# Kernel tuning notes

Hardware: AMD Instinct MI355X
Metric: run time of the kernel (lower is better)

Reference implementation:

```python
import jax, jax.numpy as jnp
import numpy as np

D_MODEL = 1024
N_HEADS = 16
HEAD_DIM = D_MODEL // N_HEADS
SCALE = float(np.sqrt(HEAD_DIM))


def setup_inputs() -> dict:
    key = jax.random.key(0)
    ks = jax.random.split(key, 12)
    B, S, D = 4, 2048, D_MODEL
    std = 1.0 / np.sqrt(D)
    inp = {
        "query": jax.random.normal(ks[0], (B, S, D), jnp.float32),
        "key": jax.random.normal(ks[1], (B, S, D), jnp.float32),
        "value": jax.random.normal(ks[2], (B, S, D), jnp.float32),
        "wq_w": jax.random.normal(ks[3], (D, D), jnp.float32) * std,
        "wq_b": jnp.zeros((D,), jnp.float32),
        "wk_w": jax.random.normal(ks[4], (D, D), jnp.float32) * std,
        "wk_b": jnp.zeros((D,), jnp.float32),
        "wv_w": jax.random.normal(ks[5], (D, D), jnp.float32) * std,
        "wv_b": jnp.zeros((D,), jnp.float32),
        "fc_w": jax.random.normal(ks[6], (D, D), jnp.float32) * std,
        "fc_b": jnp.zeros((D,), jnp.float32),
    }
    return inp


def reference(query, key, value, wq_w, wq_b, wk_w, wk_b, wv_w, wv_b, fc_w, fc_b):
    B, S, D = query.shape
    H, Hd = N_HEADS, HEAD_DIM
    # QKV projections (torch Linear: x @ W.T + b)
    Q = query @ wq_w.T + wq_b
    K = key @ wk_w.T + wk_b
    V = value @ wv_w.T + wv_b
    # [B, H, S, Hd]
    Q = Q.reshape(B, S, H, Hd).transpose(0, 2, 1, 3)
    K = K.reshape(B, S, H, Hd).transpose(0, 2, 1, 3)
    V = V.reshape(B, S, H, Hd).transpose(0, 2, 1, 3)
    energy = jnp.einsum("bhqd,bhkd->bhqk", Q, K) / SCALE
    attention = jax.nn.softmax(energy, axis=-1)  # dropout=0 (eval)
    weighted = jnp.einsum("bhqk,bhkd->bhqd", attention, V)
    weighted = weighted.transpose(0, 2, 1, 3).reshape(B, S, D)
    output = weighted @ fc_w.T + fc_b
    return (output, attention)
```

## Files before the change

### kernel.cpp

```cpp
#include <hip/hip_runtime.h>
#include <hip/hip_bf16.h>
#include <math.h>

typedef __attribute__((ext_vector_type(8))) short short8;
typedef __attribute__((ext_vector_type(4))) short short4v;
typedef __attribute__((ext_vector_type(4))) float float4v;
typedef __attribute__((ext_vector_type(2))) unsigned int uint2v;

#define GLD_LDS(g, l) __builtin_amdgcn_global_load_lds( \
    (const __attribute__((address_space(1))) void*)(g), \
    (__attribute__((address_space(3))) void*)(l), 16, 0, 0)

__device__ __forceinline__ short f2bf(float x) {
  __hip_bfloat16 h = __float2bfloat16(x);
  return __builtin_bit_cast(short, h);
}

__device__ __forceinline__ float fexp2(float x) {
  return __builtin_amdgcn_exp2f(x);
}

__global__ __launch_bounds__(256) void cast3(
    const float4v* __restrict__ in0, const float4v* __restrict__ in1,
    const float4v* __restrict__ in2,
    short4v* __restrict__ o0, short4v* __restrict__ o1, short4v* __restrict__ o2,
    int n4)
{
  const float4v* in = blockIdx.y == 0 ? in0 : blockIdx.y == 1 ? in1 : in2;
  short4v* out = blockIdx.y == 0 ? o0 : blockIdx.y == 1 ? o1 : o2;
  int i = blockIdx.x * 256 + threadIdx.x;
  if (i < n4) {
    float4v v = in[i];
    short4v o;
    o[0] = f2bf(v[0]); o[1] = f2bf(v[1]); o[2] = f2bf(v[2]); o[3] = f2bf(v[3]);
    out[i] = o;
  }
}

__global__ __launch_bounds__(256) void cast4(
    const float4v* __restrict__ in0, const float4v* __restrict__ in1,
    const float4v* __restrict__ in2, const float4v* __restrict__ in3,
    short4v* __restrict__ o0, short4v* __restrict__ o1,
    short4v* __restrict__ o2, short4v* __restrict__ o3,
    int n4)
{
  const float4v* in = blockIdx.y == 0 ? in0 : blockIdx.y == 1 ? in1
                    : blockIdx.y == 2 ? in2 : in3;
  short4v* out = blockIdx.y == 0 ? o0 : blockIdx.y == 1 ? o1
               : blockIdx.y == 2 ? o2 : o3;
  int i = blockIdx.x * 256 + threadIdx.x;
  if (i < n4) {
    float4v v = in[i];
    short4v o;
    o[0] = f2bf(v[0]); o[1] = f2bf(v[1]); o[2] = f2bf(v[2]); o[3] = f2bf(v[3]);
    out[i] = o;
  }
}

template<int MODE>
__global__ __launch_bounds__(256) void gemm_bt(
    const short* __restrict__ A0, const short* __restrict__ B0,
    const float* __restrict__ bias0, void* __restrict__ Cv0,
    const short* __restrict__ A1, const short* __restrict__ B1,
    const float* __restrict__ bias1, void* __restrict__ Cv1,
    int M, int N, int K)
{
  const short* A = blockIdx.z ? A1 : A0;
  const short* B = blockIdx.z ? B1 : B0;
  const float* bias = blockIdx.z ? bias1 : bias0;
  void* Cv = blockIdx.z ? Cv1 : Cv0;

  __shared__ short As[2][128 * 64];
  __shared__ short Bs[2][128 * 64];
  const int tid = threadIdx.x;
  const int w = tid >> 6, lane = tid & 63;
  const int g = lane >> 4, cc = lane & 15;
  const int m0 = blockIdx.x * 128, n0 = blockIdx.y * 128;
  const int wr = (w >> 1) * 64, wc = (w & 1) * 64;

  float4v acc[4][4];
#pragma unroll
  for (int mi = 0; mi < 4; ++mi)
#pragma unroll
    for (int ni = 0; ni < 4; ++ni)
      acc[mi][ni] = (float4v){0.f, 0.f, 0.f, 0.f};

  const int cbase0 = w * 64;
  const int row_l[4] = {(cbase0 + lane) >> 3, (256 + cbase0 + lane) >> 3,
                        (512 + cbase0 + lane) >> 3, (768 + cbase0 + lane) >> 3};
  const int col_l = (lane & 7) * 8;

  auto stage = [&](int buf, int k0) {
#pragma unroll
    for (int i = 0; i < 4; ++i) {
      int cbase = i * 256 + cbase0;
      GLD_LDS(A + (long)(m0 + row_l[i]) * K + k0 + col_l, &As[buf][cbase * 8]);
      GLD_LDS(B + (long)(n0 + row_l[i]) * K + k0 + col_l, &Bs[buf][cbase * 8]);
    }
  };
  auto compute = [&](int buf) {
#pragma unroll
    for (int ks = 0; ks < 2; ++ks) {
      short8 af[4], bfr[4];
#pragma unroll
      for (int mi = 0; mi < 4; ++mi)
        af[mi] = *(const short8*)&As[buf][(wr + mi * 16 + cc) * 64 + ks * 32 + g * 8];
#pragma unroll
      for (int ni = 0; ni < 4; ++ni)
        bfr[ni] = *(const short8*)&Bs[buf][(wc + ni * 16 + cc) * 64 + ks * 32 + g * 8];
#pragma unroll
      for (int mi = 0; mi < 4; ++mi)
#pragma unroll
        for (int ni = 0; ni < 4; ++ni)
          acc[mi][ni] = __builtin_amdgcn_mfma_f32_16x16x32_bf16(
              af[mi], bfr[ni], acc[mi][ni], 0, 0, 0);
    }
  };

  stage(0, 0);
  __syncthreads();
#pragma unroll 1
  for (int k0 = 0; k0 < K; k0 += 128) {
    stage(1, k0 + 64);
    compute(0);
    __syncthreads();
    if (k0 + 128 < K) stage(0, k0 + 128);
    compute(1);
    __syncthreads();
  }

#pragma unroll
  for (int mi = 0; mi < 4; ++mi) {
#pragma unroll
    for (int ni = 0; ni < 4; ++ni) {
      int mb = m0 + wr + mi * 16 + g * 4;
      int nn = n0 + wc + ni * 16 + cc;
      float4v v = acc[mi][ni];
      if constexpr (MODE == 0) {
        float bb = bias[nn];
        __hip_bfloat16* C = (__hip_bfloat16*)Cv;
#pragma unroll
        for (int r = 0; r < 4; ++r)
          C[(long)(mb + r) * N + nn] = __float2bfloat16(v[r] + bb);
      } else if constexpr (MODE == 1) {
        __hip_bfloat16* C = (__hip_bfloat16*)Cv;
        long base = (long)(nn >> 11) * 2097152 + (nn & 2047);
#pragma unroll
        for (int r = 0; r < 4; ++r)
          C[(long)(mb + r) * 2048 + base] = __float2bfloat16(v[r] + bias[mb + r]);
      } else {
        float bb = bias[nn];
        float* C = (float*)Cv;
#pragma unroll
        for (int r = 0; r < 4; ++r)
          C[(long)(mb + r) * N + nn] = v[r] + bb;
      }
    }
  }
}

__global__ __launch_bounds__(256) void attn_fwd(
    const short* __restrict__ Qb, const short* __restrict__ Kb,
    const short* __restrict__ VTb, float* __restrict__ attn_out,
    __hip_bfloat16* __restrict__ Wout)
{
  __shared__ short plds[4][32][152];
  const int S = 2048, D = 1024;
  const int bid = blockIdx.x;
  const int x = bid >> 7, r = bid & 127;
  const int bh = x * 8 + (r & 7), qi = r >> 3;
  const int b = bh >> 4, h = bh & 15;
  const int tid = threadIdx.x, w = tid >> 6, lane = tid & 63;
  const int g = lane >> 4, cc = lane & 15;
  const int q0 = qi * 128 + w * 32;

  const short* Qp = Qb + (long)b * S * D + h * 64;
  const short* Kp = Kb + (long)b * S * D + h * 64;
  const short* Vt = VTb + (long)bh * 64 * S;

  short8 qf[2][2];
#pragma unroll
  for (int mi = 0; mi < 2; ++mi)
#pragma unroll
    for (int ks = 0; ks < 2; ++ks)
      qf[mi][ks] = *(const short8*)(Qp + (long)(q0 + mi * 16 + cc) * D + ks * 32 + g * 8);

  float l[2] = {0.f, 0.f};
  const float C2 = 0.18033688011112042f;

#pragma unroll 1
  for (int kt = 0; kt < S; kt += 128) {
    short8 kfA[2][4], kfB[2][4];
#pragma unroll
    for (int ks = 0; ks < 2; ++ks)
#pragma unroll
      for (int ni = 0; ni < 4; ++ni) {
        kfA[ks][ni] = *(const short8*)(Kp + (long)(kt + ni * 16 + cc) * D + ks * 32 + g * 8);
        kfB[ks][ni] = *(const short8*)(Kp + (long)(kt + 64 + ni * 16 + cc) * D + ks * 32 + g * 8);
      }
    float4v eA[2][4], eB[2][4];
#pragma unroll
    for (int mi = 0; mi < 2; ++mi)
#pragma unroll
      for (int ni = 0; ni < 4; ++ni) {
        eA[mi][ni] = (float4v){0.f, 0.f, 0.f, 0.f};
        eB[mi][ni] = (float4v){0.f, 0.f, 0.f, 0.f};
      }
#pragma unroll
    for (int ks = 0; ks < 2; ++ks)
#pragma unroll
      for (int mi = 0; mi < 2; ++mi)
#pragma unroll
        for (int ni = 0; ni < 4; ++ni) {
          eA[mi][ni] = __builtin_amdgcn_mfma_f32_16x16x32_bf16(
              kfA[ks][ni], qf[mi][ks], eA[mi][ni], 0, 0, 0);
          eB[mi][ni] = __builtin_amdgcn_mfma_f32_16x16x32_bf16(
              kfB[ks][ni], qf[mi][ks], eB[mi][ni], 0, 0, 0);
        }
#pragma unroll
    for (int mi = 0; mi < 2; ++mi)
#pragma unroll
      for (int ni = 0; ni < 4; ++ni)
#pragma unroll
        for (int r2 = 0; r2 < 4; ++r2) {
          l[mi] += fexp2(eA[mi][ni][r2] * C2);
          l[mi] += fexp2(eB[mi][ni][r2] * C2);
        }
  }
  float lrl[2];
#pragma unroll
  for (int mi = 0; mi < 2; ++mi) {
    float s = l[mi];
    s += __shfl_xor(s, 16);
    s += __shfl_xor(s, 32);
    lrl[mi] = -__log2f(s);
  }

  float4v Wacc[2][4];
#pragma unroll
  for (int mi = 0; mi < 2; ++mi)
#pragma unroll
    for (int ni = 0; ni < 4; ++ni) Wacc[mi][ni] = (float4v){0.f, 0.f, 0.f, 0.f};

  float* Arow = attn_out + (long)bh * S * S;
#pragma unroll 1
  for (int kt = 0; kt < S; kt += 128) {
    short8 kfA[2][4], kfB[2][4];
#pragma unroll
    for (int ks = 0; ks < 2; ++ks)
#pragma unroll
      for (int ni = 0; ni < 4; ++ni) {
        kfA[ks][ni] = *(const short8*)(Kp + (long)(kt + ni * 16 + cc) * D + ks * 32 + g * 8);
        kfB[ks][ni] = *(const short8*)(Kp + (long)(kt + 64 + ni * 16 + cc) * D + ks * 32 + g * 8);
      }
    float4v eA[2][4], eB[2][4];
#pragma unroll
    for (int mi = 0; mi < 2; ++mi)
#pragma unroll
      for (int ni = 0; ni < 4; ++ni) {
        eA[mi][ni] = (float4v){0.f, 0.f, 0.f, 0.f};
        eB[mi][ni] = (float4v){0.f, 0.f, 0.f, 0.f};
      }
#pragma unroll
    for (int ks = 0; ks < 2; ++ks)
#pragma unroll
      for (int mi = 0; mi < 2; ++mi)
#pragma unroll
        for (int ni = 0; ni < 4; ++ni) {
          eA[mi][ni] = __builtin_amdgcn_mfma_f32_16x16x32_bf16(
              kfA[ks][ni], qf[mi][ks], eA[mi][ni], 0, 0, 0);
          eB[mi][ni] = __builtin_amdgcn_mfma_f32_16x16x32_bf16(
              kfB[ks][ni], qf[mi][ks], eB[mi][ni], 0, 0, 0);
        }
#pragma unroll
    for (int mi = 0; mi < 2; ++mi) {
#pragma unroll
      for (int ni = 0; ni < 4; ++ni) {
        short4v pbA, pbB;
#pragma unroll
        for (int r2 = 0; r2 < 4; ++r2) {
          pbA[r2] = f2bf(fexp2(__builtin_fmaf(eA[mi][ni][r2], C2, lrl[mi])));
          pbB[r2] = f2bf(fexp2(__builtin_fmaf(eB[mi][ni][r2], C2, lrl[mi])));
        }
        *(short4v*)&plds[w][mi * 16 + cc][ni * 16 + g * 4] = pbA;
        *(short4v*)&plds[w][mi * 16 + cc][72 + ni * 16 + g * 4] = pbB;
      }
    }
#pragma unroll
    for (int j = 0; j < 8; ++j) {
      uint2v uA = *(const uint2v*)&plds[w][j * 4 + g][cc * 4];
      uint2v uB = *(const uint2v*)&plds[w][j * 4 + g][72 + cc * 4];
      float4v pA, pB;
      pA[0] = __builtin_bit_cast(float, uA[0] << 16);
      pA[1] = __builtin_bit_cast(float, uA[0] & 0xffff0000u);
      pA[2] = __builtin_bit_cast(float, uA[1] << 16);
      pA[3] = __builtin_bit_cast(float, uA[1] & 0xffff0000u);
      pB[0] = __builtin_bit_cast(float, uB[0] << 16);
      pB[1] = __builtin_bit_cast(float, uB[0] & 0xffff0000u);
      pB[2] = __builtin_bit_cast(float, uB[1] << 16);
      pB[3] = __builtin_bit_cast(float, uB[1] & 0xffff0000u);
      float* rowp = Arow + (long)(q0 + j * 4 + g) * S + cc * 4;
      __builtin_nontemporal_store(pA, (float4v*)(rowp + kt));
      __builtin_nontemporal_store(pB, (float4v*)(rowp + kt + 64));
    }
#pragma unroll
    for (int ks = 0; ks < 2; ++ks) {
      short8 paA[2], paB[2], vfA[4], vfB[4];
#pragma unroll
      for (int mi = 0; mi < 2; ++mi) {
        paA[mi] = *(const short8*)&plds[w][mi * 16 + cc][ks * 32 + g * 8];
        paB[mi] = *(const short8*)&plds[w][mi * 16 + cc][72 + ks * 32 + g * 8];
      }
#pragma unroll
      for (int ni = 0; ni < 4; ++ni) {
        vfA[ni] = *(const short8*)(Vt + (long)(ni * 16 + cc) * S + kt + ks * 32 + g * 8);
        vfB[ni] = *(const short8*)(Vt + (long)(ni * 16 + cc) * S + kt + 64 + ks * 32 + g * 8);
      }
#pragma unroll
      for (int mi = 0; mi < 2; ++mi)
#pragma unroll
        for (int ni = 0; ni < 4; ++ni) {
          Wacc[mi][ni] = __builtin_amdgcn_mfma_f32_16x16x32_bf16(
              paA[mi], vfA[ni], Wacc[mi][ni], 0, 0, 0);
          Wacc[mi][ni] = __builtin_amdgcn_mfma_f32_16x16x32_bf16(
              paB[mi], vfB[ni], Wacc[mi][ni], 0, 0, 0);
        }
    }
  }

#pragma unroll
  for (int mi = 0; mi < 2; ++mi)
#pragma unroll
    for (int ni = 0; ni < 4; ++ni)
#pragma unroll
      for (int r2 = 0; r2 < 4; ++r2)
        Wout[(long)(b * S + q0 + mi * 16 + g * 4 + r2) * D + h * 64 + ni * 16 + cc] =
            __float2bfloat16(Wacc[mi][ni][r2]);
}

extern "C" void kernel_launch(void* const* d_in, const int* in_sizes, int n_in,
                              void* d_out, int out_size, void* d_ws, size_t ws_size,
                              hipStream_t stream) {
  const float* query = (const float*)d_in[0];
  const float* key   = (const float*)d_in[1];
  const float* value = (const float*)d_in[2];
  const float* wq_w  = (const float*)d_in[3];
  const float* wq_b  = (const float*)d_in[4];
  const float* wk_w  = (const float*)d_in[5];
  const float* wk_b  = (const float*)d_in[6];
  const float* wv_w  = (const float*)d_in[7];
  const float* wv_b  = (const float*)d_in[8];
  const float* fc_w  = (const float*)d_in[9];
  const float* fc_b  = (const float*)d_in[10];

  char* ws = (char*)d_ws;
  short* Qb  = (short*)(ws);
  short* Kb  = (short*)(ws + 16777216);
  short* VT  = (short*)(ws + 33554432);
  short* Wq  = (short*)(ws + 50331648);
  short* Wk  = (short*)(ws + 52428800);
  short* Wv  = (short*)(ws + 54525952);
  short* Wfc = (short*)(ws + 56623104);
  short* Xq  = (short*)(ws + 58720256);
  short* Xk  = (short*)(ws + 75497472);
  short* Xv  = (short*)(ws + 92274688);
  short* Wgt = Xq;

  float* out0 = (float*)d_out;
  float* attn_out = out0 + 8388608;

  cast3<<<dim3(8192, 3), 256, 0, stream>>>(
      (const float4v*)query, (const float4v*)key, (const float4v*)value,
      (short4v*)Xq, (short4v*)Xk, (short4v*)Xv, 2097152);
  cast4<<<dim3(1024, 4), 256, 0, stream>>>(
      (const float4v*)wq_w, (const float4v*)wk_w, (const float4v*)wv_w,
      (const float4v*)fc_w,
      (short4v*)Wq, (short4v*)Wk, (short4v*)Wv, (short4v*)Wfc, 262144);

  gemm_bt<0><<<dim3(64, 8, 2), 256, 0, stream>>>(
      Xq, Wq, wq_b, Qb, Xk, Wk, wk_b, Kb, 8192, 1024, 1024);
  gemm_bt<1><<<dim3(8, 64), 256, 0, stream>>>(
      Wv, Xv, wv_b, VT, Wv, Xv, wv_b, VT, 1024, 8192, 1024);

  attn_fwd<<<dim3(1024), 256, 0, stream>>>(Qb, Kb, VT, attn_out,
                                           (__hip_bfloat16*)Wgt);

  gemm_bt<2><<<dim3(64, 8), 256, 0, stream>>>(
      Wgt, Wfc, fc_b, out0, Wgt, Wfc, fc_b, out0, 8192, 1024, 1024);
}
```

Baseline: 517.8 us.

## Software-pipeline attention loop: overlap QK^T/softmax of tile i with PV of tile i-1

Replaces the 128-key tile loop, which handled two 64-key halves together, with a 64-key loop of 33 iterations. The probability tile is double-buffered in LDS, so each iteration computes QK^T, exp and the attention store for the current tile while running the PV MFMAs on the previous tile. The aim is to let the exp/VALU work and the global stores overlap with matrix-core work. The cost is an extra prologue and epilogue iteration with branches, plus different register pressure from the unroll-by-2.

```diff
diff --git a/kernel.cpp b/kernel.cpp
--- a/kernel.cpp
+++ b/kernel.cpp
@@ -243,88 +243,74 @@
     for (int ni = 0; ni < 4; ++ni) Wacc[mi][ni] = (float4v){0.f, 0.f, 0.f, 0.f};
 
   float* Arow = attn_out + (long)bh * S * S;
-#pragma unroll 1
-  for (int kt = 0; kt < S; kt += 128) {
-    short8 kfA[2][4], kfB[2][4];
-#pragma unroll
-    for (int ks = 0; ks < 2; ++ks)
-#pragma unroll
-      for (int ni = 0; ni < 4; ++ni) {
-        kfA[ks][ni] = *(const short8*)(Kp + (long)(kt + ni * 16 + cc) * D + ks * 32 + g * 8);
-        kfB[ks][ni] = *(const short8*)(Kp + (long)(kt + 64 + ni * 16 + cc) * D + ks * 32 + g * 8);
-      }
-    float4v eA[2][4], eB[2][4];
-#pragma unroll
-    for (int mi = 0; mi < 2; ++mi)
-#pragma unroll
-      for (int ni = 0; ni < 4; ++ni) {
-        eA[mi][ni] = (float4v){0.f, 0.f, 0.f, 0.f};
-        eB[mi][ni] = (float4v){0.f, 0.f, 0.f, 0.f};
-      }
-#pragma unroll
-    for (int ks = 0; ks < 2; ++ks)
+#pragma unroll 2
+  for (int it = 0; it < 33; ++it) {
+    const int kt = it * 64;
+    const int cur = (it & 1) * 72;
+    const int prv = ((it ^ 1) & 1) * 72;
+
+    if (it < 32) {
+      short8 kf[2][4];
+#pragma unroll
+      for (int ks = 0; ks < 2; ++ks)
+#pragma unroll
+        for (int ni = 0; ni < 4; ++ni)
+          kf[ks][ni] = *(const short8*)(Kp + (long)(kt + ni * 16 + cc) * D + ks * 32 + g * 8);
+      float4v e[2][4];
 #pragma unroll
       for (int mi = 0; mi < 2; ++mi)
 #pragma unroll
+        for (int ni = 0; ni < 4; ++ni) e[mi][ni] = (float4v){0.f, 0.f, 0.f, 0.f};
+#pragma unroll
+      for (int ks = 0; ks < 2; ++ks)
+#pragma unroll
+        for (int mi = 0; mi < 2; ++mi)
+#pragma unroll
+          for (int ni = 0; ni < 4; ++ni)
+            e[mi][ni] = __builtin_amdgcn_mfma_f32_16x16x32_bf16(
+                kf[ks][ni], qf[mi][ks], e[mi][ni], 0, 0, 0);
+#pragma unroll
+      for (int mi = 0; mi < 2; ++mi) {
+#pragma unroll
         for (int ni = 0; ni < 4; ++ni) {
-          eA[mi][ni] = __builtin_amdgcn_mfma_f32_16x16x32_bf16(
-              kfA[ks][ni], qf[mi][ks], eA[mi][ni], 0, 0, 0);
-          eB[mi][ni] = __builtin_amdgcn_mfma_f32_16x16x32_bf16(
-              kfB[ks][ni], qf[mi][ks], eB[mi][ni], 0, 0, 0);
+          short4v pb;
+#pragma unroll
+          for (int r2 = 0; r2 < 4; ++r2)
+            pb[r2] = f2bf(fexp2(__builtin_fmaf(e[mi][ni][r2], C2, lrl[mi])));
+          *(short4v*)&plds[w][mi * 16 + cc][cur + ni * 16 + g * 4] = pb;
         }
-#pragma unroll
-    for (int mi = 0; mi < 2; ++mi) {
-#pragma unroll
-      for (int ni = 0; ni < 4; ++ni) {
-        short4v pbA, pbB;
-#pragma unroll
-        for (int r2 = 0; r2 < 4; ++r2) {
-          pbA[r2] = f2bf(fexp2(__builtin_fmaf(eA[mi][ni][r2], C2, lrl[mi])));
-          pbB[r2] = f2bf(fexp2(__builtin_fmaf(eB[mi][ni][r2], C2, lrl[mi])));
-        }
-        *(short4v*)&plds[w][mi * 16 + cc][ni * 16 + g * 4] = pbA;
-        *(short4v*)&plds[w][mi * 16 + cc][72 + ni * 16 + g * 4] = pbB;
-      }
-    }
-#pragma unroll
-    for (int j = 0; j < 8; ++j) {
-      uint2v uA = *(const uint2v*)&plds[w][j * 4 + g][cc * 4];
-      uint2v uB = *(const uint2v*)&plds[w][j * 4 + g][72 + cc * 4];
-      float4v pA, pB;
-      pA[0] = __builtin_bit_cast(float, uA[0] << 16);
-      pA[1] = __builtin_bit_cast(float, uA[0] & 0xffff0000u);
-      pA[2] = __builtin_bit_cast(float, uA[1] << 16);
-      pA[3] = __builtin_bit_cast(float, uA[1] & 0xffff0000u);
-      pB[0] = __builtin_bit_cast(float, uB[0] << 16);
-      pB[1] = __builtin_bit_cast(float, uB[0] & 0xffff0000u);
-      pB[2] = __builtin_bit_cast(float, uB[1] << 16);
-      pB[3] = __builtin_bit_cast(float, uB[1] & 0xffff0000u);
-      float* rowp = Arow + (long)(q0 + j * 4 + g) * S + cc * 4;
-      __builtin_nontemporal_store(pA, (float4v*)(rowp + kt));
-      __builtin_nontemporal_store(pB, (float4v*)(rowp + kt + 64));
-    }
-#pragma unroll
-    for (int ks = 0; ks < 2; ++ks) {
-      short8 paA[2], paB[2], vfA[4], vfB[4];
-#pragma unroll
-      for (int mi = 0; mi < 2; ++mi) {
-        paA[mi] = *(const short8*)&plds[w][mi * 16 + cc][ks * 32 + g * 8];
-        paB[mi] = *(const short8*)&plds[w][mi * 16 + cc][72 + ks * 32 + g * 8];
-      }
-#pragma unroll
-      for (int ni = 0; ni < 4; ++ni) {
-        vfA[ni] = *(const short8*)(Vt + (long)(ni * 16 + cc) * S + kt + ks * 32 + g * 8);
-        vfB[ni] = *(const short8*)(Vt + (long)(ni * 16 + cc) * S + kt + 64 + ks * 32 + g * 8);
-      }
-#pragma unroll
-      for (int mi = 0; mi < 2; ++mi)
-#pragma unroll
-        for (int ni = 0; ni < 4; ++ni) {
-          Wacc[mi][ni] = __builtin_amdgcn_mfma_f32_16x16x32_bf16(
-              paA[mi], vfA[ni], Wacc[mi][ni], 0, 0, 0);
-          Wacc[mi][ni] = __builtin_amdgcn_mfma_f32_16x16x32_bf16(
-              paB[mi], vfB[ni], Wacc[mi][ni], 0, 0, 0);
-        }
+      }
+#pragma unroll
+      for (int j = 0; j < 8; ++j) {
+        uint2v u = *(const uint2v*)&plds[w][j * 4 + g][cur + cc * 4];
+        float4v pv4;
+        pv4[0] = __builtin_bit_cast(float, u[0] << 16);
+        pv4[1] = __builtin_bit_cast(float, u[0] & 0xffff0000u);
+        pv4[2] = __builtin_bit_cast(float, u[1] << 16);
+        pv4[3] = __builtin_bit_cast(float, u[1] & 0xffff0000u);
+        __builtin_nontemporal_store(
+            pv4, (float4v*)(Arow + (long)(q0 + j * 4 + g) * S + kt + cc * 4));
+      }
+    }
+
+    if (it > 0) {
+      const int ktp = (it - 1) * 64;
+#pragma unroll
+      for (int ks = 0; ks < 2; ++ks) {
+        short8 pa[2], vf[4];
+#pragma unroll
+        for (int mi = 0; mi < 2; ++mi)
+          pa[mi] = *(const short8*)&plds[w][mi * 16 + cc][prv + ks * 32 + g * 8];
+#pragma unroll
+        for (int ni = 0; ni < 4; ++ni)
+          vf[ni] = *(const short8*)(Vt + (long)(ni * 16 + cc) * S + ktp + ks * 32 + g * 8);
+#pragma unroll
+        for (int mi = 0; mi < 2; ++mi)
+#pragma unroll
+          for (int ni = 0; ni < 4; ++ni)
+            Wacc[mi][ni] = __builtin_amdgcn_mfma_f32_16x16x32_bf16(
+                pa[mi], vf[ni], Wacc[mi][ni], 0, 0, 0);
+      }
     }
   }
 
```

Result: no change. 527.1 us (+1.8%).
